# Kernel tuning notes

Measured on AMD Instinct MI355X. Metric: run time of the kernel, lower is better.

The kernel has to match this reference:

```python
import jax, jax.numpy as jnp
import numpy as np

DIM = 1024
NUM_HEADS = 16
HEAD_DIM = DIM // NUM_HEADS


def setup_inputs() -> dict:
    key = jax.random.key(0)
    ks = jax.random.split(key, 8)
    B, N = 4, 1024
    x = jax.random.normal(ks[0], (B, N, DIM), dtype=jnp.float32)
    # RoPE tables per position, broadcast over batch/heads
    pos = jnp.arange(N, dtype=jnp.float32)[:, None]
    inv_freq = 1.0 / (10000.0 ** (jnp.arange(0, HEAD_DIM, 2, dtype=jnp.float32) / HEAD_DIM))
    ang = pos * inv_freq[None, :]                      # [N, D/2]
    ang = jnp.concatenate([ang, ang], axis=-1)          # [N, D]
    cos, sin = jnp.cos(ang), jnp.sin(ang)
    s_in = 1.0 / np.sqrt(DIM)
    qkv_w = jax.random.normal(ks[1], (3 * DIM, DIM), dtype=jnp.float32) * s_in
    qkv_b = jax.random.normal(ks[2], (3 * DIM,), dtype=jnp.float32) * 0.02
    proj_w = jax.random.normal(ks[3], (DIM, DIM), dtype=jnp.float32) * s_in
    proj_b = jax.random.normal(ks[4], (DIM,), dtype=jnp.float32) * 0.02
    return {"x": x, "cos": cos, "sin": sin, "qkv_w": qkv_w, "qkv_b": qkv_b,
            "proj_w": proj_w, "proj_b": proj_b}


def _rotate_half(t):
    t1, t2 = jnp.split(t, 2, axis=-1)
    return jnp.concatenate([-t2, t1], axis=-1)


def reference(x, cos, sin, qkv_w, qkv_b, proj_w, proj_b):
    B, N, C = x.shape
    H, D = NUM_HEADS, HEAD_DIM
    scale = D ** -0.5
    qkv = x @ qkv_w.T + qkv_b                           # [B, N, 3C]
    qkv = qkv.reshape(B, N, 3, H, D).transpose(2, 0, 3, 1, 4)  # [3, B, H, N, D]
    q, k, v = qkv[0], qkv[1], qkv[2]
    q = q * cos + _rotate_half(q) * sin                 # cos/sin [N, D] broadcast
    k = k * cos + _rotate_half(k) * sin
    attn = jnp.einsum('bhnd,bhmd->bhnm', q, k) * scale  # [B, H, N, N]
    attn = jax.nn.softmax(attn, axis=-1)
    out = jnp.einsum('bhnm,bhmd->bhnd', attn, v)        # [B, H, N, D]
    out = out.transpose(0, 2, 1, 3).reshape(B, N, C)
    return out @ proj_w.T + proj_b
```

## Files before the change

### kernel.cpp

```cpp
#include <hip/hip_runtime.h>

typedef __attribute__((ext_vector_type(8))) short bf16x8;
typedef __attribute__((ext_vector_type(4))) float f32x4;
typedef __attribute__((ext_vector_type(4))) unsigned short us4;

#define LOG2E 1.44269504088896f
#define GP(p) (const __attribute__((address_space(1))) void*)(p)
#define LP(p) (__attribute__((address_space(3))) void*)(p)

__device__ inline unsigned short f2bf(float f) {
    unsigned u = __float_as_uint(f);
    u += 0x7fffu + ((u >> 16) & 1u);
    return (unsigned short)(u >> 16);
}

__device__ inline unsigned cvt_pk_bf16(float lo, float hi) {
    unsigned r;
    asm("v_cvt_pk_bf16_f32 %0, %1, %2" : "=v"(r) : "v"(lo), "v"(hi));
    return r;
}

__global__ void cvt_kernel(const float* __restrict__ src, unsigned short* __restrict__ dst, int n) {
    int i = (blockIdx.x * blockDim.x + threadIdx.x) * 4;
    const int stride = gridDim.x * blockDim.x * 4;
    for (; i < n; i += stride) {
        const float4 v = *reinterpret_cast<const float4*>(src + i);
        us4 o;
        o.x = f2bf(v.x); o.y = f2bf(v.y); o.z = f2bf(v.z); o.w = f2bf(v.w);
        *reinterpret_cast<us4*>(dst + i) = o;
    }
}

__device__ inline void gemm_mainloop_db(const unsigned short* __restrict__ A,
                                        const unsigned short* __restrict__ Bw,
                                        unsigned short* As, unsigned short* Bs,
                                        int tm, int tn, f32x4 (&acc)[4][4]) {
    const int K = 1024;
    const int tid = threadIdx.x;
    const int lane = tid & 63;
    const int wv = tid >> 6;
    const int wr = wv >> 1, wc = wv & 1;
    const int lr = lane & 15, lg = lane >> 4;

    const int c1 = tid, c2 = tid + 256;
    const int r1 = c1 >> 2, r2 = c2 >> 2;
    const int g1 = ((c1 & 3) ^ ((r1 >> 1) & 3)) * 8;
    const int g2 = ((c2 & 3) ^ ((r2 >> 1) & 3)) * 8;
    const unsigned short* Ag1 = A + (size_t)(tm * 128 + r1) * K + g1;
    const unsigned short* Ag2 = A + (size_t)(tm * 128 + r2) * K + g2;
    const unsigned short* Bg1 = Bw + (size_t)(tn * 128 + r1) * K + g1;
    const unsigned short* Bg2 = Bw + (size_t)(tn * 128 + r2) * K + g2;

    const int rs = (lr >> 1) & 3;
    const int rdA = (wr * 64 + lr) * 32 + ((0 ^ rs) * 8);
    const int rdB = (wc * 64 + lr) * 32;

    auto STAGE = [&](int buf, int k0) {
        __builtin_amdgcn_global_load_lds(GP(Ag1 + k0), LP(As + buf * 4096 + c1 * 8), 16, 0, 0);
        __builtin_amdgcn_global_load_lds(GP(Ag2 + k0), LP(As + buf * 4096 + c2 * 8), 16, 0, 0);
        __builtin_amdgcn_global_load_lds(GP(Bg1 + k0), LP(Bs + buf * 4096 + c1 * 8), 16, 0, 0);
        __builtin_amdgcn_global_load_lds(GP(Bg2 + k0), LP(Bs + buf * 4096 + c2 * 8), 16, 0, 0);
    };

    STAGE(0, 0);
    for (int t = 0; t < 32; t++) {
        const int buf = t & 1;
        if (t < 31) {
            STAGE(buf ^ 1, (t + 1) * 32);
            asm volatile("s_waitcnt vmcnt(4)" ::: "memory");
        } else {
            asm volatile("s_waitcnt vmcnt(0)" ::: "memory");
        }
        __builtin_amdgcn_s_barrier();
        __builtin_amdgcn_sched_barrier(0);

        bf16x8 af[4], bfv[4];
#pragma unroll
        for (int i = 0; i < 4; i++) {
            const int sl = (lg ^ rs) * 8;
            af[i]  = *reinterpret_cast<const bf16x8*>(As + buf * 4096 + (wr * 64 + i * 16 + lr) * 32 + sl);
            bfv[i] = *reinterpret_cast<const bf16x8*>(Bs + buf * 4096 + (wc * 64 + i * 16 + lr) * 32 + sl);
        }
        __builtin_amdgcn_s_setprio(1);
#pragma unroll
        for (int i = 0; i < 4; i++)
#pragma unroll
            for (int j = 0; j < 4; j++)
                acc[i][j] = __builtin_amdgcn_mfma_f32_16x16x32_bf16(af[i], bfv[j], acc[i][j], 0, 0, 0);
        __builtin_amdgcn_s_setprio(0);
        __builtin_amdgcn_s_barrier();
        __builtin_amdgcn_sched_barrier(0);
    }
}

__global__ __launch_bounds__(256, 3) void gemm_qkv_kernel(
        const unsigned short* __restrict__ A, const unsigned short* __restrict__ Bw,
        const float* __restrict__ bias, const float* __restrict__ cosT, const float* __restrict__ sinT,
        unsigned short* __restrict__ Qb, unsigned short* __restrict__ Kb, unsigned short* __restrict__ Vt) {
    __shared__ __align__(16) unsigned short As[2 * 4096];
    __shared__ __align__(16) unsigned short Bs[2 * 4096];
    const int tid = threadIdx.x;
    const int lane = tid & 63;
    const int wv = tid >> 6;
    const int wr = wv >> 1, wc = wv & 1;
    const int tm = blockIdx.y, tn = blockIdx.x;
    const int lr = lane & 15, lg = lane >> 4;

    f32x4 acc[4][4];
#pragma unroll
    for (int i = 0; i < 4; i++)
#pragma unroll
        for (int j = 0; j < 4; j++)
#pragma unroll
            for (int q = 0; q < 4; q++) acc[i][j][q] = 0.f;

    gemm_mainloop_db(A, Bw, As, Bs, tm, tn, acc);

    const int cbase = tn * 128 + wc * 64;
    const int sec = cbase >> 10;
    const int h = (cbase & 1023) >> 6;
    float bias_c[4];
#pragma unroll
    for (int j = 0; j < 4; j++) bias_c[j] = bias[cbase + j * 16 + lr];

    if (sec == 2) {
#pragma unroll
        for (int i = 0; i < 4; i++) {
            const int m0 = tm * 128 + wr * 64 + i * 16 + lg * 4;
            const int b = m0 >> 10, n0 = m0 & 1023;
#pragma unroll
            for (int j = 0; j < 4; j++) {
                const int d = j * 16 + lr;
                us4 pk;
                pk.x = f2bf(acc[i][j][0] + bias_c[j]); pk.y = f2bf(acc[i][j][1] + bias_c[j]);
                pk.z = f2bf(acc[i][j][2] + bias_c[j]); pk.w = f2bf(acc[i][j][3] + bias_c[j]);
                *reinterpret_cast<us4*>(Vt + ((size_t)((b * 16 + h) * 64 + d)) * 1024 + n0) = pk;
            }
        }
    } else {
#pragma unroll
        for (int i = 0; i < 4; i++) {
#pragma unroll
            for (int r = 0; r < 4; r++) {
                const int m = tm * 128 + wr * 64 + i * 16 + lg * 4 + r;
                const int b = m >> 10, n = m & 1023;
                float vals[4];
#pragma unroll
                for (int j = 0; j < 4; j++) vals[j] = acc[i][j][r] + bias_c[j];
#pragma unroll
                for (int j = 0; j < 4; j++) {
                    const int d = j * 16 + lr;
                    const float c = cosT[n * 64 + d];
                    const float s = sinT[n * 64 + d];
                    const float pr = vals[j ^ 2];
                    float outv = vals[j] * c + (d < 32 ? -pr : pr) * s;
                    if (sec == 0) outv *= 0.125f * LOG2E;
                    unsigned short* dst = (sec == 0) ? Qb : Kb;
                    dst[((size_t)((b * 16 + h) * 1024 + n)) * 64 + d] = f2bf(outv);
                }
            }
        }
    }
}

__global__ __launch_bounds__(256, 4) void attn_kernel(
        const unsigned short* __restrict__ Qb, const unsigned short* __restrict__ Kb,
        const unsigned short* __restrict__ Vt, unsigned short* __restrict__ AO) {
    __shared__ __align__(16) unsigned short KVs[2][8192];
    const int tid = threadIdx.x, lane = tid & 63, wv = tid >> 6;
    const int bh = blockIdx.x, qt = blockIdx.y;
    const int qbase = qt * 64 + wv * 16;
    const unsigned short* Qp = Qb + (size_t)bh * 65536;
    const unsigned short* Kp = Kb + (size_t)bh * 65536;
    const unsigned short* Vp = Vt + (size_t)bh * 65536;
    const int lr = lane & 15, lg = lane >> 4;
    const int koff = (lr >> 2) * 8 + (lr & 3);

    const int s1 = tid, s2 = tid + 256;
    const int r1 = s1 >> 3, r2 = s2 >> 3;
    const int sc1 = (s1 & 7) ^ ((r1 & 3) | ((r1 >> 1) & 4));
    const int sc2 = (s2 & 7) ^ ((r2 & 3) | ((r2 >> 1) & 4));
    const unsigned short* Ks1 = Kp + r1 * 64 + sc1 * 8;
    const unsigned short* Ks2 = Kp + r2 * 64 + sc2 * 8;
    const unsigned short* Vs1 = Vp + r1 * 1024 + sc1 * 8;
    const unsigned short* Vs2 = Vp + r2 * 1024 + sc2 * 8;

    auto STAGE = [&](int buf, int kt) {
        unsigned short* base = &KVs[buf][0];
        __builtin_amdgcn_global_load_lds(GP(Ks1 + kt * 64), LP(base + s1 * 8), 16, 0, 0);
        __builtin_amdgcn_global_load_lds(GP(Ks2 + kt * 64), LP(base + s2 * 8), 16, 0, 0);
        __builtin_amdgcn_global_load_lds(GP(Vs1 + kt), LP(base + 4096 + s1 * 8), 16, 0, 0);
        __builtin_amdgcn_global_load_lds(GP(Vs2 + kt), LP(base + 4096 + s2 * 8), 16, 0, 0);
    };

    bf16x8 qfr[2];
#pragma unroll
    for (int kc = 0; kc < 2; kc++)
        qfr[kc] = *reinterpret_cast<const bf16x8*>(Qp + (qbase + lr) * 64 + kc * 32 + lg * 8);

    f32x4 o[4];
    float m_ = -1e30f, l_ = 0.f;
#pragma unroll
    for (int df = 0; df < 4; df++)
#pragma unroll
        for (int r = 0; r < 4; r++) o[df][r] = 0.f;

    STAGE(0, 0);
    for (int t = 0; t < 16; t++) {
        const int cur = t & 1;
        if (t < 15) {
            STAGE(cur ^ 1, (t + 1) * 64);
            asm volatile("s_waitcnt vmcnt(4)" ::: "memory");
        } else {
            asm volatile("s_waitcnt vmcnt(0)" ::: "memory");
        }
        __builtin_amdgcn_s_barrier();
        __builtin_amdgcn_sched_barrier(0);

        const unsigned short* Kl = &KVs[cur][0];
        const unsigned short* Vl = &KVs[cur][4096];

        f32x4 s[4];
#pragma unroll
        for (int kf = 0; kf < 4; kf++)
#pragma unroll
            for (int r = 0; r < 4; r++) s[kf][r] = 0.f;
        __builtin_amdgcn_s_setprio(1);
#pragma unroll
        for (int kc = 0; kc < 2; kc++) {
#pragma unroll
            for (int kf = 0; kf < 4; kf++) {
                const int row = ((kf >> 1) << 5) + ((kf & 1) << 2) + koff;
                const int col = (kc * 4 + lg) ^ ((row & 3) | ((row >> 1) & 4));
                const bf16x8 kfr = *reinterpret_cast<const bf16x8*>(Kl + row * 64 + col * 8);
                s[kf] = __builtin_amdgcn_mfma_f32_16x16x32_bf16(kfr, qfr[kc], s[kf], 0, 0, 0);
            }
        }
        __builtin_amdgcn_s_setprio(0);

        float mx = s[0][0];
#pragma unroll
        for (int kf = 0; kf < 4; kf++)
#pragma unroll
            for (int r = 0; r < 4; r++) mx = fmaxf(mx, s[kf][r]);
        if (!__all(mx <= m_ + 11.0f)) {
            mx = fmaxf(mx, __shfl_xor(mx, 16, 64));
            mx = fmaxf(mx, __shfl_xor(mx, 32, 64));
            const float mnew = fmaxf(m_, mx);
            const float fsc = exp2f(m_ - mnew);
            m_ = mnew;
            l_ *= fsc;
#pragma unroll
            for (int df = 0; df < 4; df++)
#pragma unroll
                for (int r = 0; r < 4; r++) o[df][r] *= fsc;
        }
        float rs = 0.f;
#pragma unroll
        for (int kf = 0; kf < 4; kf++)
#pragma unroll
            for (int r = 0; r < 4; r++) {
                const float p = exp2f(s[kf][r] - m_);
                s[kf][r] = p;
                rs += p;
            }
        l_ += rs;

#pragma unroll
        for (int kc = 0; kc < 2; kc++) {
            union { bf16x8 v; unsigned u[4]; } pk;
            pk.u[0] = cvt_pk_bf16(s[2 * kc][0], s[2 * kc][1]);
            pk.u[1] = cvt_pk_bf16(s[2 * kc][2], s[2 * kc][3]);
            pk.u[2] = cvt_pk_bf16(s[2 * kc + 1][0], s[2 * kc + 1][1]);
            pk.u[3] = cvt_pk_bf16(s[2 * kc + 1][2], s[2 * kc + 1][3]);
            const bf16x8 pfr = pk.v;
            __builtin_amdgcn_s_setprio(1);
#pragma unroll
            for (int df = 0; df < 4; df++) {
                const int vrow = df * 16 + lr;
                const int vcol = (kc * 4 + lg) ^ ((vrow & 3) | ((vrow >> 1) & 4));
                const bf16x8 vfr = *reinterpret_cast<const bf16x8*>(Vl + vrow * 64 + vcol * 8);
                o[df] = __builtin_amdgcn_mfma_f32_16x16x32_bf16(vfr, pfr, o[df], 0, 0, 0);
            }
            __builtin_amdgcn_s_setprio(0);
        }
        __builtin_amdgcn_s_barrier();
    }

    const int b = bh >> 4, h = bh & 15;
    float lt = l_;
    lt += __shfl_xor(lt, 16, 64);
    lt += __shfl_xor(lt, 32, 64);
    const float rinv = 1.f / lt;
    const int q = qbase + lr;
#pragma unroll
    for (int df = 0; df < 4; df++) {
        us4 pk;
        pk.x = f2bf(o[df][0] * rinv); pk.y = f2bf(o[df][1] * rinv);
        pk.z = f2bf(o[df][2] * rinv); pk.w = f2bf(o[df][3] * rinv);
        *reinterpret_cast<us4*>(AO + (size_t)(b * 1024 + q) * 1024 + h * 64 + df * 16 + lg * 4) = pk;
    }
}

__global__ __launch_bounds__(256, 3) void gemm_proj_kernel(
        const unsigned short* __restrict__ A, const unsigned short* __restrict__ Bw,
        const float* __restrict__ bias, float* __restrict__ out) {
    __shared__ __align__(16) unsigned short As[2 * 4096];
    __shared__ __align__(16) unsigned short Bs[2 * 4096];
    const int tid = threadIdx.x;
    const int lane = tid & 63;
    const int wv = tid >> 6;
    const int wr = wv >> 1, wc = wv & 1;
    const int tm = blockIdx.y, tn = blockIdx.x;
    const int lr = lane & 15, lg = lane >> 4;

    f32x4 acc[4][4];
#pragma unroll
    for (int i = 0; i < 4; i++)
#pragma unroll
        for (int j = 0; j < 4; j++)
#pragma unroll
            for (int q = 0; q < 4; q++) acc[i][j][q] = 0.f;

    gemm_mainloop_db(A, Bw, As, Bs, tm, tn, acc);

#pragma unroll
    for (int i = 0; i < 4; i++)
#pragma unroll
        for (int j = 0; j < 4; j++)
#pragma unroll
            for (int r = 0; r < 4; r++) {
                const int row = tm * 128 + wr * 64 + i * 16 + lg * 4 + r;
                const int col = tn * 128 + wc * 64 + j * 16 + lr;
                out[(size_t)row * 1024 + col] = acc[i][j][r] + bias[col];
            }
}

extern "C" void kernel_launch(void* const* d_in, const int* in_sizes, int n_in,
                              void* d_out, int out_size, void* d_ws, size_t ws_size,
                              hipStream_t stream) {
    const float* x      = (const float*)d_in[0];
    const float* cosT   = (const float*)d_in[1];
    const float* sinT   = (const float*)d_in[2];
    const float* qkv_w  = (const float*)d_in[3];
    const float* qkv_b  = (const float*)d_in[4];
    const float* proj_w = (const float*)d_in[5];
    const float* proj_b = (const float*)d_in[6];
    float* out = (float*)d_out;

    char* ws = (char*)d_ws;
    unsigned short* xb    = (unsigned short*)(ws);
    unsigned short* wqkv  = (unsigned short*)(ws + (8u << 20));
    unsigned short* wproj = (unsigned short*)(ws + (14u << 20));
    unsigned short* Qb    = (unsigned short*)(ws + (16u << 20));
    unsigned short* Kb    = (unsigned short*)(ws + (24u << 20));
    unsigned short* Vt    = (unsigned short*)(ws + (32u << 20));
    unsigned short* AO    = (unsigned short*)(ws + (40u << 20));

    cvt_kernel<<<2048, 256, 0, stream>>>(x, xb, 4096 * 1024);
    cvt_kernel<<<2048, 256, 0, stream>>>(qkv_w, wqkv, 3072 * 1024);
    cvt_kernel<<<1024, 256, 0, stream>>>(proj_w, wproj, 1024 * 1024);
    gemm_qkv_kernel<<<dim3(24, 32), 256, 0, stream>>>(xb, wqkv, qkv_b, cosT, sinT, Qb, Kb, Vt);
    attn_kernel<<<dim3(64, 16), 256, 0, stream>>>(Qb, Kb, Vt, AO);
    gemm_proj_kernel<<<dim3(8, 32), 256, 0, stream>>>(AO, wproj, proj_b, out);
}
```

Before: 108.3 us.

## Merge conversion kernels, double query rows per attention wave, widen proj K-tile

Folds the three fp32-to-bf16 conversion launches into one kernel that covers all three buffers. The attention kernel now runs 2 waves per block, each handling 32 query rows, so every K/V fragment read from LDS feeds two MFMAs. The output projection GEMM gets its own mainloop with a 64-wide K tile, twice the LDS and fewer barriers. The cost is more registers per wave, fewer waves in flight for attention, and lower occupancy (2 blocks) for the projection.

Measured after the change: 105.6 us. -2.4%, faster.

```diff
diff --git a/kernel.cpp b/kernel.cpp
--- a/kernel.cpp
+++ b/kernel.cpp
@@ -20,14 +20,20 @@
     return r;
 }
 
-__global__ void cvt_kernel(const float* __restrict__ src, unsigned short* __restrict__ dst, int n) {
-    int i = (blockIdx.x * blockDim.x + threadIdx.x) * 4;
-    const int stride = gridDim.x * blockDim.x * 4;
-    for (; i < n; i += stride) {
-        const float4 v = *reinterpret_cast<const float4*>(src + i);
+__global__ void cvt3_kernel(const float* __restrict__ x, const float* __restrict__ qw,
+                            const float* __restrict__ pw,
+                            unsigned short* __restrict__ xb, unsigned short* __restrict__ wqkv,
+                            unsigned short* __restrict__ wproj) {
+    const int nthreads = gridDim.x * blockDim.x;
+    for (int i = blockIdx.x * blockDim.x + threadIdx.x; i < 2097152; i += nthreads) {
+        const float* src; unsigned short* dst; int off;
+        if (i < 1048576)      { src = x;  dst = xb;    off = i; }
+        else if (i < 1835008) { src = qw; dst = wqkv;  off = i - 1048576; }
+        else                  { src = pw; dst = wproj; off = i - 1835008; }
+        const float4 v = *reinterpret_cast<const float4*>(src + off * 4);
         us4 o;
         o.x = f2bf(v.x); o.y = f2bf(v.y); o.z = f2bf(v.z); o.w = f2bf(v.w);
-        *reinterpret_cast<us4*>(dst + i) = o;
+        *reinterpret_cast<us4*>(dst + off * 4) = o;
     }
 }
 
@@ -52,8 +58,6 @@
     const unsigned short* Bg2 = Bw + (size_t)(tn * 128 + r2) * K + g2;
 
     const int rs = (lr >> 1) & 3;
-    const int rdA = (wr * 64 + lr) * 32 + ((0 ^ rs) * 8);
-    const int rdB = (wc * 64 + lr) * 32;
 
     auto STAGE = [&](int buf, int k0) {
         __builtin_amdgcn_global_load_lds(GP(Ag1 + k0), LP(As + buf * 4096 + c1 * 8), 16, 0, 0);
@@ -163,54 +167,66 @@
     }
 }
 
-__global__ __launch_bounds__(256, 4) void attn_kernel(
+__global__ __launch_bounds__(128, 2) void attn_kernel(
         const unsigned short* __restrict__ Qb, const unsigned short* __restrict__ Kb,
         const unsigned short* __restrict__ Vt, unsigned short* __restrict__ AO) {
     __shared__ __align__(16) unsigned short KVs[2][8192];
     const int tid = threadIdx.x, lane = tid & 63, wv = tid >> 6;
     const int bh = blockIdx.x, qt = blockIdx.y;
-    const int qbase = qt * 64 + wv * 16;
+    const int qbase = qt * 64 + wv * 32;
     const unsigned short* Qp = Qb + (size_t)bh * 65536;
     const unsigned short* Kp = Kb + (size_t)bh * 65536;
     const unsigned short* Vp = Vt + (size_t)bh * 65536;
     const int lr = lane & 15, lg = lane >> 4;
     const int koff = (lr >> 2) * 8 + (lr & 3);
 
-    const int s1 = tid, s2 = tid + 256;
-    const int r1 = s1 >> 3, r2 = s2 >> 3;
-    const int sc1 = (s1 & 7) ^ ((r1 & 3) | ((r1 >> 1) & 4));
-    const int sc2 = (s2 & 7) ^ ((r2 & 3) | ((r2 >> 1) & 4));
-    const unsigned short* Ks1 = Kp + r1 * 64 + sc1 * 8;
-    const unsigned short* Ks2 = Kp + r2 * 64 + sc2 * 8;
-    const unsigned short* Vs1 = Vp + r1 * 1024 + sc1 * 8;
-    const unsigned short* Vs2 = Vp + r2 * 1024 + sc2 * 8;
+    const unsigned short* Ksrc[4];
+    const unsigned short* Vsrc[4];
+    int dstoff[4];
+#pragma unroll
+    for (int j = 0; j < 4; j++) {
+        const int c = tid + j * 128;
+        const int row = c >> 3, sl = c & 7;
+        const int gs = (sl ^ ((row & 3) | ((row >> 1) & 4))) * 8;
+        Ksrc[j] = Kp + row * 64 + gs;
+        Vsrc[j] = Vp + row * 1024 + gs;
+        dstoff[j] = c * 8;
+    }
 
     auto STAGE = [&](int buf, int kt) {
         unsigned short* base = &KVs[buf][0];
-        __builtin_amdgcn_global_load_lds(GP(Ks1 + kt * 64), LP(base + s1 * 8), 16, 0, 0);
-        __builtin_amdgcn_global_load_lds(GP(Ks2 + kt * 64), LP(base + s2 * 8), 16, 0, 0);
-        __builtin_amdgcn_global_load_lds(GP(Vs1 + kt), LP(base + 4096 + s1 * 8), 16, 0, 0);
-        __builtin_amdgcn_global_load_lds(GP(Vs2 + kt), LP(base + 4096 + s2 * 8), 16, 0, 0);
+#pragma unroll
+        for (int j = 0; j < 4; j++)
+            __builtin_amdgcn_global_load_lds(GP(Ksrc[j] + kt * 64), LP(base + dstoff[j]), 16, 0, 0);
+#pragma unroll
+        for (int j = 0; j < 4; j++)
+            __builtin_amdgcn_global_load_lds(GP(Vsrc[j] + kt), LP(base + 4096 + dstoff[j]), 16, 0, 0);
     };
 
-    bf16x8 qfr[2];
-#pragma unroll
-    for (int kc = 0; kc < 2; kc++)
-        qfr[kc] = *reinterpret_cast<const bf16x8*>(Qp + (qbase + lr) * 64 + kc * 32 + lg * 8);
-
-    f32x4 o[4];
-    float m_ = -1e30f, l_ = 0.f;
+    bf16x8 qfr[2][2];
+#pragma unroll
+    for (int qf = 0; qf < 2; qf++)
+#pragma unroll
+        for (int kc = 0; kc < 2; kc++)
+            qfr[qf][kc] = *reinterpret_cast<const bf16x8*>(Qp + (qbase + qf * 16 + lr) * 64 + kc * 32 + lg * 8);
+
+    f32x4 o[4][2];
+    float m_[2], l_[2];
 #pragma unroll
     for (int df = 0; df < 4; df++)
 #pragma unroll
-        for (int r = 0; r < 4; r++) o[df][r] = 0.f;
+        for (int qf = 0; qf < 2; qf++)
+#pragma unroll
+            for (int r = 0; r < 4; r++) o[df][qf][r] = 0.f;
+    m_[0] = m_[1] = -1e30f;
+    l_[0] = l_[1] = 0.f;
 
     STAGE(0, 0);
     for (int t = 0; t < 16; t++) {
         const int cur = t & 1;
         if (t < 15) {
             STAGE(cur ^ 1, (t + 1) * 64);
-            asm volatile("s_waitcnt vmcnt(4)" ::: "memory");
+            asm volatile("s_waitcnt vmcnt(8)" ::: "memory");
         } else {
             asm volatile("s_waitcnt vmcnt(0)" ::: "memory");
         }
@@ -220,11 +236,13 @@
         const unsigned short* Kl = &KVs[cur][0];
         const unsigned short* Vl = &KVs[cur][4096];
 
-        f32x4 s[4];
+        f32x4 s[4][2];
 #pragma unroll
         for (int kf = 0; kf < 4; kf++)
 #pragma unroll
-            for (int r = 0; r < 4; r++) s[kf][r] = 0.f;
+            for (int qf = 0; qf < 2; qf++)
+#pragma unroll
+                for (int r = 0; r < 4; r++) s[kf][qf][r] = 0.f;
         __builtin_amdgcn_s_setprio(1);
 #pragma unroll
         for (int kc = 0; kc < 2; kc++) {
@@ -233,54 +251,63 @@
                 const int row = ((kf >> 1) << 5) + ((kf & 1) << 2) + koff;
                 const int col = (kc * 4 + lg) ^ ((row & 3) | ((row >> 1) & 4));
                 const bf16x8 kfr = *reinterpret_cast<const bf16x8*>(Kl + row * 64 + col * 8);
-                s[kf] = __builtin_amdgcn_mfma_f32_16x16x32_bf16(kfr, qfr[kc], s[kf], 0, 0, 0);
+                s[kf][0] = __builtin_amdgcn_mfma_f32_16x16x32_bf16(kfr, qfr[0][kc], s[kf][0], 0, 0, 0);
+                s[kf][1] = __builtin_amdgcn_mfma_f32_16x16x32_bf16(kfr, qfr[1][kc], s[kf][1], 0, 0, 0);
             }
         }
         __builtin_amdgcn_s_setprio(0);
 
-        float mx = s[0][0];
-#pragma unroll
-        for (int kf = 0; kf < 4; kf++)
-#pragma unroll
-            for (int r = 0; r < 4; r++) mx = fmaxf(mx, s[kf][r]);
-        if (!__all(mx <= m_ + 11.0f)) {
-            mx = fmaxf(mx, __shfl_xor(mx, 16, 64));
-            mx = fmaxf(mx, __shfl_xor(mx, 32, 64));
-            const float mnew = fmaxf(m_, mx);
-            const float fsc = exp2f(m_ - mnew);
-            m_ = mnew;
-            l_ *= fsc;
-#pragma unroll
-            for (int df = 0; df < 4; df++)
-#pragma unroll
-                for (int r = 0; r < 4; r++) o[df][r] *= fsc;
-        }
-        float rs = 0.f;
-#pragma unroll
-        for (int kf = 0; kf < 4; kf++)
-#pragma unroll
-            for (int r = 0; r < 4; r++) {
-                const float p = exp2f(s[kf][r] - m_);
-                s[kf][r] = p;
-                rs += p;
-            }
-        l_ += rs;
+#pragma unroll
+        for (int qf = 0; qf < 2; qf++) {
+            float mx = s[0][qf][0];
+#pragma unroll
+            for (int kf = 0; kf < 4; kf++)
+#pragma unroll
+                for (int r = 0; r < 4; r++) mx = fmaxf(mx, s[kf][qf][r]);
+            if (!__all(mx <= m_[qf] + 11.0f)) {
+                mx = fmaxf(mx, __shfl_xor(mx, 16, 64));
+                mx = fmaxf(mx, __shfl_xor(mx, 32, 64));
+                const float mnew = fmaxf(m_[qf], mx);
+                const float fsc = exp2f(m_[qf] - mnew);
+                m_[qf] = mnew;
+                l_[qf] *= fsc;
+#pragma unroll
+                for (int df = 0; df < 4; df++)
+#pragma unroll
+                    for (int r = 0; r < 4; r++) o[df][qf][r] *= fsc;
+            }
+            float rs = 0.f;
+#pragma unroll
+            for (int kf = 0; kf < 4; kf++)
+#pragma unroll
+                for (int r = 0; r < 4; r++) {
+                    const float p = exp2f(s[kf][qf][r] - m_[qf]);
+                    s[kf][qf][r] = p;
+                    rs += p;
+                }
+            l_[qf] += rs;
+        }
 
 #pragma unroll
         for (int kc = 0; kc < 2; kc++) {
-            union { bf16x8 v; unsigned u[4]; } pk;
-            pk.u[0] = cvt_pk_bf16(s[2 * kc][0], s[2 * kc][1]);
-            pk.u[1] = cvt_pk_bf16(s[2 * kc][2], s[2 * kc][3]);
-            pk.u[2] = cvt_pk_bf16(s[2 * kc + 1][0], s[2 * kc + 1][1]);
-            pk.u[3] = cvt_pk_bf16(s[2 * kc + 1][2], s[2 * kc + 1][3]);
-            const bf16x8 pfr = pk.v;
+            bf16x8 pfr[2];
+#pragma unroll
+            for (int qf = 0; qf < 2; qf++) {
+                union { bf16x8 v; unsigned u[4]; } pk;
+                pk.u[0] = cvt_pk_bf16(s[2 * kc][qf][0], s[2 * kc][qf][1]);
+                pk.u[1] = cvt_pk_bf16(s[2 * kc][qf][2], s[2 * kc][qf][3]);
+                pk.u[2] = cvt_pk_bf16(s[2 * kc + 1][qf][0], s[2 * kc + 1][qf][1]);
+                pk.u[3] = cvt_pk_bf16(s[2 * kc + 1][qf][2], s[2 * kc + 1][qf][3]);
+                pfr[qf] = pk.v;
+            }
             __builtin_amdgcn_s_setprio(1);
 #pragma unroll
             for (int df = 0; df < 4; df++) {
                 const int vrow = df * 16 + lr;
                 const int vcol = (kc * 4 + lg) ^ ((vrow & 3) | ((vrow >> 1) & 4));
                 const bf16x8 vfr = *reinterpret_cast<const bf16x8*>(Vl + vrow * 64 + vcol * 8);
-                o[df] = __builtin_amdgcn_mfma_f32_16x16x32_bf16(vfr, pfr, o[df], 0, 0, 0);
+                o[df][0] = __builtin_amdgcn_mfma_f32_16x16x32_bf16(vfr, pfr[0], o[df][0], 0, 0, 0);
+                o[df][1] = __builtin_amdgcn_mfma_f32_16x16x32_bf16(vfr, pfr[1], o[df][1], 0, 0, 0);
             }
             __builtin_amdgcn_s_setprio(0);
         }
@@ -288,25 +315,28 @@
     }
 
     const int b = bh >> 4, h = bh & 15;
-    float lt = l_;
-    lt += __shfl_xor(lt, 16, 64);
-    lt += __shfl_xor(lt, 32, 64);
-    const float rinv = 1.f / lt;
-    const int q = qbase + lr;
-#pragma unroll
-    for (int df = 0; df < 4; df++) {
-        us4 pk;
-        pk.x = f2bf(o[df][0] * rinv); pk.y = f2bf(o[df][1] * rinv);
-        pk.z = f2bf(o[df][2] * rinv); pk.w = f2bf(o[df][3] * rinv);
-        *reinterpret_cast<us4*>(AO + (size_t)(b * 1024 + q) * 1024 + h * 64 + df * 16 + lg * 4) = pk;
-    }
-}
-
-__global__ __launch_bounds__(256, 3) void gemm_proj_kernel(
+#pragma unroll
+    for (int qf = 0; qf < 2; qf++) {
+        float lt = l_[qf];
+        lt += __shfl_xor(lt, 16, 64);
+        lt += __shfl_xor(lt, 32, 64);
+        const float rinv = 1.f / lt;
+        const int q = qbase + qf * 16 + lr;
+#pragma unroll
+        for (int df = 0; df < 4; df++) {
+            us4 pk;
+            pk.x = f2bf(o[df][qf][0] * rinv); pk.y = f2bf(o[df][qf][1] * rinv);
+            pk.z = f2bf(o[df][qf][2] * rinv); pk.w = f2bf(o[df][qf][3] * rinv);
+            *reinterpret_cast<us4*>(AO + (size_t)(b * 1024 + q) * 1024 + h * 64 + df * 16 + lg * 4) = pk;
+        }
+    }
+}
+
+__global__ __launch_bounds__(256, 2) void gemm_proj_kernel(
         const unsigned short* __restrict__ A, const unsigned short* __restrict__ Bw,
         const float* __restrict__ bias, float* __restrict__ out) {
-    __shared__ __align__(16) unsigned short As[2 * 4096];
-    __shared__ __align__(16) unsigned short Bs[2 * 4096];
+    __shared__ __align__(16) unsigned short As[2 * 8192];
+    __shared__ __align__(16) unsigned short Bs[2 * 8192];
     const int tid = threadIdx.x;
     const int lane = tid & 63;
     const int wv = tid >> 6;
@@ -314,6 +344,19 @@
     const int tm = blockIdx.y, tn = blockIdx.x;
     const int lr = lane & 15, lg = lane >> 4;
 
+    const unsigned short* Ag[4];
+    const unsigned short* Bg[4];
+    int doff[4];
+#pragma unroll
+    for (int j = 0; j < 4; j++) {
+        const int c = tid + j * 256;
+        const int row = c >> 3, sl = c & 7;
+        const int gs = (sl ^ ((row & 3) | ((row >> 1) & 4))) * 8;
+        Ag[j] = A + (size_t)(tm * 128 + row) * 1024 + gs;
+        Bg[j] = Bw + (size_t)(tn * 128 + row) * 1024 + gs;
+        doff[j] = c * 8;
+    }
+
     f32x4 acc[4][4];
 #pragma unroll
     for (int i = 0; i < 4; i++)
@@ -322,7 +365,51 @@
 #pragma unroll
             for (int q = 0; q < 4; q++) acc[i][j][q] = 0.f;
 
-    gemm_mainloop_db(A, Bw, As, Bs, tm, tn, acc);
+    auto STAGE = [&](int buf, int k0) {
+#pragma unroll
+        for (int j = 0; j < 4; j++)
+            __builtin_amdgcn_global_load_lds(GP(Ag[j] + k0), LP(As + buf * 8192 + doff[j]), 16, 0, 0);
+#pragma unroll
+        for (int j = 0; j < 4; j++)
+            __builtin_amdgcn_global_load_lds(GP(Bg[j] + k0), LP(Bs + buf * 8192 + doff[j]), 16, 0, 0);
+    };
+
+    STAGE(0, 0);
+    for (int t = 0; t < 16; t++) {
+        const int buf = t & 1;
+        if (t < 15) {
+            STAGE(buf ^ 1, (t + 1) * 64);
+            asm volatile("s_waitcnt vmcnt(8)" ::: "memory");
+        } else {
+            asm volatile("s_waitcnt vmcnt(0)" ::: "memory");
+        }
+        __builtin_amdgcn_s_barrier();
+        __builtin_amdgcn_sched_barrier(0);
+
+        bf16x8 af[4][2], bfv[4][2];
+#pragma unroll
+        for (int i = 0; i < 4; i++)
+#pragma unroll
+            for (int kk = 0; kk < 2; kk++) {
+                const int ra = wr * 64 + i * 16 + lr;
+                const int rb = wc * 64 + i * 16 + lr;
+                af[i][kk]  = *reinterpret_cast<const bf16x8*>(
+                    As + buf * 8192 + ra * 64 + ((kk * 4 + lg) ^ ((ra & 3) | ((ra >> 1) & 4))) * 8);
+                bfv[i][kk] = *reinterpret_cast<const bf16x8*>(
+                    Bs + buf * 8192 + rb * 64 + ((kk * 4 + lg) ^ ((rb & 3) | ((rb >> 1) & 4))) * 8);
+            }
+        __builtin_amdgcn_s_setprio(1);
+#pragma unroll
+        for (int i = 0; i < 4; i++)
+#pragma unroll
+            for (int j = 0; j < 4; j++)
+#pragma unroll
+                for (int kk = 0; kk < 2; kk++)
+                    acc[i][j] = __builtin_amdgcn_mfma_f32_16x16x32_bf16(af[i][kk], bfv[j][kk], acc[i][j], 0, 0, 0);
+        __builtin_amdgcn_s_setprio(0);
+        __builtin_amdgcn_s_barrier();
+        __builtin_amdgcn_sched_barrier(0);
+    }
 
 #pragma unroll
     for (int i = 0; i < 4; i++)
@@ -357,10 +444,8 @@
     unsigned short* Vt    = (unsigned short*)(ws + (32u << 20));
     unsigned short* AO    = (unsigned short*)(ws + (40u << 20));
 
-    cvt_kernel<<<2048, 256, 0, stream>>>(x, xb, 4096 * 1024);
-    cvt_kernel<<<2048, 256, 0, stream>>>(qkv_w, wqkv, 3072 * 1024);
-    cvt_kernel<<<1024, 256, 0, stream>>>(proj_w, wproj, 1024 * 1024);
+    cvt3_kernel<<<2048, 256, 0, stream>>>(x, qkv_w, proj_w, xb, wqkv, wproj);
     gemm_qkv_kernel<<<dim3(24, 32), 256, 0, stream>>>(xb, wqkv, qkv_b, cosT, sinT, Qb, Kb, Vt);
-    attn_kernel<<<dim3(64, 16), 256, 0, stream>>>(Qb, Kb, Vt, AO);
+    attn_kernel<<<dim3(64, 16), 128, 0, stream>>>(Qb, Kb, Vt, AO);
     gemm_proj_kernel<<<dim3(8, 32), 256, 0, stream>>>(AO, wproj, proj_b, out);
 }
```
